# Performance work log

Hardware: AMD Instinct MI355X
Metric: run time of the kernel (lower is better)

## Reference

```python
import jax, jax.numpy as jnp
import numpy as np

D = 256      # dim_model (hardcoded in module)
H = 8        # n_head
HD = 64      # num_neuron (per-head dim)
NL = 5       # number of transformer blocks
FF = 4 * D   # FFN hidden
VOCAB = 32000
OUT = 4096
B = 32
S = 512
LN_EPS = 1e-5


def layer_norm(x, s, b):
    m = jnp.mean(x, axis=-1, keepdims=True)
    v = jnp.mean(jnp.square(x - m), axis=-1, keepdims=True)
    return (x - m) * jax.lax.rsqrt(v + LN_EPS) * s + b


def setup_inputs() -> dict:
    key = jax.random.key(0)
    ks = jax.random.split(key, 12)
    sd = 0.02
    return {
        "x": jax.random.randint(ks[0], (B, S), 0, VOCAB),
        "emb": jax.random.normal(ks[1], (VOCAB, D), jnp.float32) * sd,
        "wq": jax.random.normal(ks[2], (NL, D, H * HD), jnp.float32) * sd,
        "bq": jnp.zeros((NL, H * HD), jnp.float32),
        "wk": jax.random.normal(ks[3], (NL, D, H * HD), jnp.float32) * sd,
        "bk": jnp.zeros((NL, H * HD), jnp.float32),
        "wv": jax.random.normal(ks[4], (NL, D, H * HD), jnp.float32) * sd,
        "bv": jnp.zeros((NL, H * HD), jnp.float32),
        "wo": jax.random.normal(ks[5], (NL, H * HD, D), jnp.float32) * sd,
        "bo": jnp.zeros((NL, D), jnp.float32),
        "ln1_s": jnp.ones((NL, D), jnp.float32),
        "ln1_b": jnp.zeros((NL, D), jnp.float32),
        "w1": jax.random.normal(ks[6], (NL, D, FF), jnp.float32) * sd,
        "b1": jnp.zeros((NL, FF), jnp.float32),
        "w2": jax.random.normal(ks[7], (NL, FF, D), jnp.float32) * sd,
        "b2": jnp.zeros((NL, D), jnp.float32),
        "ln2_s": jnp.ones((NL, D), jnp.float32),
        "ln2_b": jnp.zeros((NL, D), jnp.float32),
        "ow": jax.random.normal(ks[8], (D, OUT), jnp.float32) * sd,
        "ob": jnp.zeros((OUT,), jnp.float32),
    }


def positional_encoding(seq_len):
    pos = jnp.arange(seq_len, dtype=jnp.float32)[:, None]          # [S,1]
    div = 10000.0 ** (jnp.arange(0, D, 2, dtype=jnp.float32) / D)  # [D/2]
    ang = pos / div                                                # [S,D/2]
    pe = jnp.zeros((seq_len, D), jnp.float32)
    pe = pe.at[:, 0::2].set(jnp.sin(ang))
    pe = pe.at[:, 1::2].set(jnp.cos(ang))
    return pe


def reference(x, emb, wq, bq, wk, bk, wv, bv, wo, bo,
              ln1_s, ln1_b, w1, b1, w2, b2, ln2_s, ln2_b, ow, ob):
    Bx, Sx = x.shape
    h = emb[x] + positional_encoding(Sx)[None]          # [B,S,D]
    causal = jnp.tril(jnp.ones((Sx, Sx), bool))         # [S,S]
    scale = 1.0 / jnp.sqrt(jnp.float32(HD))
    for i in range(NL):
        q = (h @ wq[i] + bq[i]).reshape(Bx, Sx, H, HD)
        k = (h @ wk[i] + bk[i]).reshape(Bx, Sx, H, HD)
        v = (h @ wv[i] + bv[i]).reshape(Bx, Sx, H, HD)
        scores = jnp.einsum('bqhd,bkhd->bhqk', q, k) * scale
        scores = jnp.where(causal, scores, -jnp.inf)
        attn_w = jax.nn.softmax(scores, axis=-1)
        o = jnp.einsum('bhqk,bkhd->bqhd', attn_w, v).reshape(Bx, Sx, H * HD)
        attn = o @ wo[i] + bo[i]
        h = layer_norm(h + attn, ln1_s[i], ln1_b[i])
        ff = jax.nn.relu(h @ w1[i] + b1[i]) @ w2[i] + b2[i]
        h = layer_norm(h + ff, ln2_s[i], ln2_b[i])
    return h @ ow + ob
```

## Files before the change

kernel.cpp:

```cpp
#include <hip/hip_runtime.h>

#define BB   32
#define SS   512
#define DD   256
#define HH   8
#define HDIM 64
#define NLAYER 5
#define FFD  1024
#define OUTD 4096
#define QN   512
#define BS   (BB*SS)

typedef short bf16x8 __attribute__((ext_vector_type(8)));
typedef float f32x4  __attribute__((ext_vector_type(4)));

__device__ __forceinline__ ushort f2bf(float f) {
    union { float f; unsigned u; } c; c.f = f;
    unsigned u = c.u;
    return (ushort)((u + 0x7fffu + ((u >> 16) & 1u)) >> 16);
}
__device__ __forceinline__ float bf2f(unsigned b) {
    union { unsigned u; float f; } c; c.u = b << 16;
    return c.f;
}

__global__ __launch_bounds__(256) void embed_pe_kernel(
        const int* __restrict__ x, const float* __restrict__ emb,
        float* __restrict__ h, ushort* __restrict__ hb) {
    int t = blockIdx.x;
    int d = threadIdx.x;
    int pos = t % SS;
    int tok = x[t];
    float e = emb[(size_t)tok * DD + d];
    float expo = -(float)(d & ~1) / (float)DD;
    float ang = (float)pos * powf(10000.0f, expo);
    float pe = (d & 1) ? cosf(ang) : sinf(ang);
    float val = e + pe;
    h[(size_t)t * DD + d] = val;
    hb[(size_t)t * DD + d] = f2bf(val);
}

__global__ __launch_bounds__(256) void convw_kernel(
        const float* __restrict__ W, ushort* __restrict__ Wt, int K, int N) {
    __shared__ float t[32][33];
    const int tid = threadIdx.x;
    const int tx = tid & 31, ty = tid >> 5;
    const int n0 = blockIdx.x * 32, k0 = blockIdx.y * 32;
#pragma unroll
    for (int i = 0; i < 4; ++i)
        t[ty + i * 8][tx] = W[(size_t)(k0 + ty + i * 8) * N + n0 + tx];
    __syncthreads();
#pragma unroll
    for (int i = 0; i < 4; ++i)
        Wt[(size_t)(n0 + ty + i * 8) * K + k0 + tx] = f2bf(t[tx][ty + i * 8]);
}

template<bool RELU, bool OBF>
__global__ __launch_bounds__(256) void gemm_mfma_kernel(
        const ushort* __restrict__ A, const ushort* __restrict__ Bt,
        const float* __restrict__ bias, void* __restrict__ Cout,
        int M, int N, int K) {
    __shared__ ushort sA[128 * 32];
    __shared__ ushort sB[128 * 32];

    const int tid  = threadIdx.x;
    const int lane = tid & 63;
    const int wave = tid >> 6;
    const int wr   = wave >> 1;
    const int wc   = wave & 1;
    const int fr   = lane & 15;
    const int fq   = lane >> 4;
    const int m0 = blockIdx.y * 128;
    const int n0 = blockIdx.x * 128;

    f32x4 acc[4][4];
#pragma unroll
    for (int mi = 0; mi < 4; ++mi)
#pragma unroll
        for (int ni = 0; ni < 4; ++ni)
            acc[mi][ni] = (f32x4){0.0f, 0.0f, 0.0f, 0.0f};

    for (int k0 = 0; k0 < K; k0 += 32) {
#pragma unroll
        for (int it = 0; it < 2; ++it) {
            const int gi  = tid + it * 256;
            const int row = gi >> 2, g = gi & 3;
            const int gs  = g ^ ((row >> 1) & 3);
            const uint4 av = *reinterpret_cast<const uint4*>(
                A + (size_t)(m0 + row) * K + k0 + g * 8);
            *reinterpret_cast<uint4*>(&sA[row * 32 + gs * 8]) = av;
            const uint4 bv = *reinterpret_cast<const uint4*>(
                Bt + (size_t)(n0 + row) * K + k0 + g * 8);
            *reinterpret_cast<uint4*>(&sB[row * 32 + gs * 8]) = bv;
        }
        __syncthreads();

        bf16x8 af[4], bfr[4];
#pragma unroll
        for (int mi = 0; mi < 4; ++mi) {
            const int row = wr * 64 + mi * 16 + fr;
            const int gs  = fq ^ ((row >> 1) & 3);
            af[mi] = *reinterpret_cast<const bf16x8*>(&sA[row * 32 + gs * 8]);
        }
#pragma unroll
        for (int ni = 0; ni < 4; ++ni) {
            const int row = wc * 64 + ni * 16 + fr;
            const int gs  = fq ^ ((row >> 1) & 3);
            bfr[ni] = *reinterpret_cast<const bf16x8*>(&sB[row * 32 + gs * 8]);
        }
#pragma unroll
        for (int mi = 0; mi < 4; ++mi)
#pragma unroll
            for (int ni = 0; ni < 4; ++ni)
                acc[mi][ni] = __builtin_amdgcn_mfma_f32_16x16x32_bf16(
                    af[mi], bfr[ni], acc[mi][ni], 0, 0, 0);
        __syncthreads();
    }

#pragma unroll
    for (int ni = 0; ni < 4; ++ni) {
        const int col = n0 + wc * 64 + ni * 16 + fr;
        const float bv = bias[col];
#pragma unroll
        for (int mi = 0; mi < 4; ++mi) {
#pragma unroll
            for (int r = 0; r < 4; ++r) {
                const int row = m0 + wr * 64 + mi * 16 + fq * 4 + r;
                float v = acc[mi][ni][r] + bv;
                if (RELU) v = fmaxf(v, 0.0f);
                if (OBF)
                    ((ushort*)Cout)[(size_t)row * N + col] = f2bf(v);
                else
                    ((float*)Cout)[(size_t)row * N + col] = v;
            }
        }
    }
}

__global__ __launch_bounds__(256) void flash_attn_kernel(
        const ushort* __restrict__ q, const ushort* __restrict__ k,
        const ushort* __restrict__ v, ushort* __restrict__ o) {
    const int qt  = blockIdx.x;
    const int hh  = blockIdx.y;
    const int b   = blockIdx.z;
    const int tid = threadIdx.x;
    const int l   = tid & 63;
    const int w   = tid >> 6;
    const int lf  = l & 15;
    const int lg  = l >> 4;

    __shared__ ushort Qs[64 * 64];
    __shared__ ushort Ks[64 * 64];
    __shared__ ushort Vt[64 * 64];
    __shared__ ushort Ps[64 * 64];

    const size_t qbase = ((size_t)(b * SS + qt * 64)) * QN + hh * HDIM;

#pragma unroll
    for (int it = 0; it < 2; ++it) {
        int gi = tid + it * 256;
        int row = gi >> 3, g = gi & 7;
        uint4 val = *reinterpret_cast<const uint4*>(
            q + qbase + (size_t)row * QN + g * 8);
        *reinterpret_cast<uint4*>(&Qs[row * 64 + ((g ^ (row & 7)) << 3)]) = val;
    }

    f32x4 o_acc[4];
    float m_i[4], l_i[4];
#pragma unroll
    for (int r = 0; r < 4; ++r) { m_i[r] = -3.0e38f; l_i[r] = 0.0f; }
#pragma unroll
    for (int ni = 0; ni < 4; ++ni) o_acc[ni] = (f32x4){0.f, 0.f, 0.f, 0.f};

    const int vkv  = l;
    const int vgd  = w * 2;

    for (int kt = 0; kt <= qt; ++kt) {
        const size_t kbase = ((size_t)(b * SS + kt * 64)) * QN + hh * HDIM;
#pragma unroll
        for (int it = 0; it < 2; ++it) {
            int gi = tid + it * 256;
            int row = gi >> 3, g = gi & 7;
            uint4 val = *reinterpret_cast<const uint4*>(
                k + kbase + (size_t)row * QN + g * 8);
            *reinterpret_cast<uint4*>(&Ks[row * 64 + ((g ^ (row & 7)) << 3)]) = val;
        }
#pragma unroll
        for (int sel = 0; sel < 2; ++sel) {
            const int gd = vgd + sel;
            uint4 raw = *reinterpret_cast<const uint4*>(
                v + kbase + (size_t)vkv * QN + gd * 8);
            unsigned e[4] = {raw.x, raw.y, raw.z, raw.w};
#pragma unroll
            for (int j = 0; j < 8; ++j) {
                int d = gd * 8 + j;
                ushort val = (ushort)((e[j >> 1] >> ((j & 1) * 16)) & 0xffff);
                Vt[d * 64 + (((vkv >> 3) ^ (d & 7)) << 3) + (vkv & 7)] = val;
            }
        }
        __syncthreads();

        f32x4 st[4];
#pragma unroll
        for (int ni = 0; ni < 4; ++ni) st[ni] = (f32x4){0.f, 0.f, 0.f, 0.f};
        const int arow = w * 16 + lf;
#pragma unroll
        for (int ks = 0; ks < 2; ++ks) {
            bf16x8 aq = *reinterpret_cast<const bf16x8*>(
                &Qs[arow * 64 + (((ks * 4 + lg) ^ (arow & 7)) << 3)]);
#pragma unroll
            for (int ni = 0; ni < 4; ++ni) {
                const int brow = ni * 16 + lf;
                bf16x8 bk = *reinterpret_cast<const bf16x8*>(
                    &Ks[brow * 64 + (((ks * 4 + lg) ^ (brow & 7)) << 3)]);
                st[ni] = __builtin_amdgcn_mfma_f32_16x16x32_bf16(aq, bk, st[ni], 0, 0, 0);
            }
        }
#pragma unroll
        for (int ni = 0; ni < 4; ++ni) st[ni] *= 0.125f;

        if (kt == qt) {
#pragma unroll
            for (int ni = 0; ni < 4; ++ni)
#pragma unroll
                for (int r = 0; r < 4; ++r)
                    if (16 * ni + lf > w * 16 + 4 * lg + r) st[ni][r] = -1.0e30f;
        }

#pragma unroll
        for (int r = 0; r < 4; ++r) {
            float mx = fmaxf(fmaxf(st[0][r], st[1][r]), fmaxf(st[2][r], st[3][r]));
#pragma unroll
            for (int off = 1; off < 16; off <<= 1)
                mx = fmaxf(mx, __shfl_xor(mx, off, 64));
            float mnew = fmaxf(m_i[r], mx);
            float alpha = __expf(m_i[r] - mnew);
            float sum = 0.0f;
#pragma unroll
            for (int ni = 0; ni < 4; ++ni) {
                float p = __expf(st[ni][r] - mnew);
                st[ni][r] = p;
                sum += p;
            }
#pragma unroll
            for (int off = 1; off < 16; off <<= 1)
                sum += __shfl_xor(sum, off, 64);
            m_i[r] = mnew;
            l_i[r] = l_i[r] * alpha + sum;
#pragma unroll
            for (int ni = 0; ni < 4; ++ni) o_acc[ni][r] *= alpha;
        }

#pragma unroll
        for (int r = 0; r < 4; ++r) {
            const int qr = w * 16 + 4 * lg + r;
#pragma unroll
            for (int ni = 0; ni < 4; ++ni) {
                const int kvc = 16 * ni + lf;
                Ps[qr * 64 + (((kvc >> 3) ^ (qr & 7)) << 3) + (kvc & 7)] =
                    f2bf(st[ni][r]);
            }
        }
        asm volatile("s_waitcnt lgkmcnt(0)" ::: "memory");
        __builtin_amdgcn_sched_barrier(0);

#pragma unroll
        for (int ks = 0; ks < 2; ++ks) {
            bf16x8 pa = *reinterpret_cast<const bf16x8*>(
                &Ps[arow * 64 + (((ks * 4 + lg) ^ (arow & 7)) << 3)]);
#pragma unroll
            for (int ni = 0; ni < 4; ++ni) {
                const int drow = ni * 16 + lf;
                bf16x8 vb = *reinterpret_cast<const bf16x8*>(
                    &Vt[drow * 64 + (((ks * 4 + lg) ^ (drow & 7)) << 3)]);
                o_acc[ni] = __builtin_amdgcn_mfma_f32_16x16x32_bf16(pa, vb, o_acc[ni], 0, 0, 0);
            }
        }
        __syncthreads();
    }

#pragma unroll
    for (int r = 0; r < 4; ++r) {
        const float invl = 1.0f / l_i[r];
        const int qrow = w * 16 + 4 * lg + r;
#pragma unroll
        for (int ni = 0; ni < 4; ++ni)
            o[qbase + (size_t)qrow * QN + 16 * ni + lf] =
                f2bf(o_acc[ni][r] * invl);
    }
}

__global__ __launch_bounds__(256) void add_ln_kernel(
        float* __restrict__ h, const float* __restrict__ delta,
        const float* __restrict__ sc, const float* __restrict__ bi,
        ushort* __restrict__ hb) {
    const int t = blockIdx.x;
    const int d = threadIdx.x;
    __shared__ float p1[4], p2[4];
    const size_t idx = (size_t)t * DD + d;
    float val = h[idx] + delta[idx];
    float s = val;
#pragma unroll
    for (int off = 1; off < 64; off <<= 1) s += __shfl_xor(s, off, 64);
    if ((d & 63) == 0) p1[d >> 6] = s;
    __syncthreads();
    float mean = (p1[0] + p1[1] + p1[2] + p1[3]) * (1.0f / DD);
    float dv = val - mean;
    float vs = dv * dv;
#pragma unroll
    for (int off = 1; off < 64; off <<= 1) vs += __shfl_xor(vs, off, 64);
    if ((d & 63) == 0) p2[d >> 6] = vs;
    __syncthreads();
    float inv = rsqrtf((p2[0] + p2[1] + p2[2] + p2[3]) * (1.0f / DD) + 1e-5f);
    float r = dv * inv * sc[d] + bi[d];
    h[idx] = r;
    hb[idx] = f2bf(r);
}

extern "C" void kernel_launch(void* const* d_in, const int* in_sizes, int n_in,
                              void* d_out, int out_size, void* d_ws, size_t ws_size,
                              hipStream_t stream) {
    (void)in_sizes; (void)n_in; (void)out_size; (void)ws_size;

    const int*   x    = (const int*)d_in[0];
    const float* emb  = (const float*)d_in[1];
    const float* wq   = (const float*)d_in[2];
    const float* bq   = (const float*)d_in[3];
    const float* wk   = (const float*)d_in[4];
    const float* bk   = (const float*)d_in[5];
    const float* wv   = (const float*)d_in[6];
    const float* bv   = (const float*)d_in[7];
    const float* wo   = (const float*)d_in[8];
    const float* bo   = (const float*)d_in[9];
    const float* ln1s = (const float*)d_in[10];
    const float* ln1b = (const float*)d_in[11];
    const float* w1   = (const float*)d_in[12];
    const float* b1   = (const float*)d_in[13];
    const float* w2   = (const float*)d_in[14];
    const float* b2   = (const float*)d_in[15];
    const float* ln2s = (const float*)d_in[16];
    const float* ln2b = (const float*)d_in[17];
    const float* ow   = (const float*)d_in[18];
    const float* ob   = (const float*)d_in[19];

    char* ws = (char*)d_ws;
    float*  h   = (float*)ws;   ws += (size_t)BS * DD * 4;
    ushort* hbf = (ushort*)ws;  ws += (size_t)BS * DD * 2;
    ushort* qb  = (ushort*)ws;  ws += (size_t)BS * QN * 2;
    ushort* kb  = (ushort*)ws;  ws += (size_t)BS * QN * 2;
    ushort* vb  = (ushort*)ws;  ws += (size_t)BS * QN * 2;
    float*  t2  = (float*)ws;   ws += (size_t)BS * DD * 4;
    ushort* wqt = (ushort*)ws;  ws += (size_t)NLAYER * QN * DD * 2;
    ushort* wkt = (ushort*)ws;  ws += (size_t)NLAYER * QN * DD * 2;
    ushort* wvt = (ushort*)ws;  ws += (size_t)NLAYER * QN * DD * 2;
    ushort* wot = (ushort*)ws;  ws += (size_t)NLAYER * DD * QN * 2;
    ushort* w1t = (ushort*)ws;  ws += (size_t)NLAYER * FFD * DD * 2;
    ushort* w2t = (ushort*)ws;  ws += (size_t)NLAYER * DD * FFD * 2;
    ushort* owt = (ushort*)ws;  ws += (size_t)OUTD * DD * 2;
    ushort* ao  = qb;
    ushort* ffh = kb;

    for (int i = 0; i < NLAYER; ++i) {
        convw_kernel<<<dim3(QN / 32, DD / 32), 256, 0, stream>>>(
            wq + (size_t)i * DD * QN, wqt + (size_t)i * QN * DD, DD, QN);
        convw_kernel<<<dim3(QN / 32, DD / 32), 256, 0, stream>>>(
            wk + (size_t)i * DD * QN, wkt + (size_t)i * QN * DD, DD, QN);
        convw_kernel<<<dim3(QN / 32, DD / 32), 256, 0, stream>>>(
            wv + (size_t)i * DD * QN, wvt + (size_t)i * QN * DD, DD, QN);
        convw_kernel<<<dim3(DD / 32, QN / 32), 256, 0, stream>>>(
            wo + (size_t)i * QN * DD, wot + (size_t)i * DD * QN, QN, DD);
        convw_kernel<<<dim3(FFD / 32, DD / 32), 256, 0, stream>>>(
            w1 + (size_t)i * DD * FFD, w1t + (size_t)i * FFD * DD, DD, FFD);
        convw_kernel<<<dim3(DD / 32, FFD / 32), 256, 0, stream>>>(
            w2 + (size_t)i * FFD * DD, w2t + (size_t)i * DD * FFD, FFD, DD);
    }
    convw_kernel<<<dim3(OUTD / 32, DD / 32), 256, 0, stream>>>(ow, owt, DD, OUTD);

    embed_pe_kernel<<<BS, 256, 0, stream>>>(x, emb, h, hbf);

    for (int i = 0; i < NLAYER; ++i) {
        dim3 gq(QN / 128, BS / 128);
        gemm_mfma_kernel<false, true><<<gq, 256, 0, stream>>>(
            hbf, wqt + (size_t)i * QN * DD, bq + i * QN, qb, BS, QN, DD);
        gemm_mfma_kernel<false, true><<<gq, 256, 0, stream>>>(
            hbf, wkt + (size_t)i * QN * DD, bk + i * QN, kb, BS, QN, DD);
        gemm_mfma_kernel<false, true><<<gq, 256, 0, stream>>>(
            hbf, wvt + (size_t)i * QN * DD, bv + i * QN, vb, BS, QN, DD);

        flash_attn_kernel<<<dim3(SS / 64, HH, BB), 256, 0, stream>>>(qb, kb, vb, ao);

        gemm_mfma_kernel<false, false><<<dim3(DD / 128, BS / 128), 256, 0, stream>>>(
            ao, wot + (size_t)i * DD * QN, bo + i * DD, t2, BS, DD, QN);
        add_ln_kernel<<<BS, 256, 0, stream>>>(h, t2, ln1s + i * DD, ln1b + i * DD, hbf);

        gemm_mfma_kernel<true, true><<<dim3(FFD / 128, BS / 128), 256, 0, stream>>>(
            hbf, w1t + (size_t)i * FFD * DD, b1 + i * FFD, ffh, BS, FFD, DD);
        gemm_mfma_kernel<false, false><<<dim3(DD / 128, BS / 128), 256, 0, stream>>>(
            ffh, w2t + (size_t)i * DD * FFD, b2 + i * DD, t2, BS, DD, FFD);
        add_ln_kernel<<<BS, 256, 0, stream>>>(h, t2, ln2s + i * DD, ln2b + i * DD, hbf);
    }

    gemm_mfma_kernel<false, false><<<dim3(OUTD / 128, BS / 128), 256, 0, stream>>>(
        hbf, owt, ob, (float*)d_out, BS, OUTD, DD);
}
```

Before: 1.443 ms.

## Fuse QKV GEMMs, fuse output GEMMs with add+LayerNorm, prefetch tiles, pre-transpose V

Merges the three Q/K/V projections into one GEMM launch over concatenated weights, and writes V transposed so the attention kernel can load it with vector copies instead of a scalar transpose. The Wo and W2 projections are fused with the residual add and LayerNorm in a new full-row GEMM kernel, which removes the t2 round trip and the separate add_ln launches. All GEMM and attention loops gain register prefetch of the next tile, overlapping global loads with MFMA work. The embedding now uses fast-math exp/sin/cos. The fused LN kernel runs only 256 blocks with 16 accumulators per lane, so occupancy may drop.

```diff
diff --git a/kernel.cpp b/kernel.cpp
--- a/kernel.cpp
+++ b/kernel.cpp
@@ -33,8 +33,8 @@
     int tok = x[t];
     float e = emb[(size_t)tok * DD + d];
     float expo = -(float)(d & ~1) / (float)DD;
-    float ang = (float)pos * powf(10000.0f, expo);
-    float pe = (d & 1) ? cosf(ang) : sinf(ang);
+    float ang = (float)pos * __expf(expo * 9.210340371976184f);
+    float pe = (d & 1) ? __cosf(ang) : __sinf(ang);
     float val = e + pe;
     h[(size_t)t * DD + d] = val;
     hb[(size_t)t * DD + d] = f2bf(val);
@@ -73,6 +73,10 @@
     const int m0 = blockIdx.y * 128;
     const int n0 = blockIdx.x * 128;
 
+    const int strow = tid >> 2;
+    const int stg   = tid & 3;
+    const int stgs  = stg ^ ((strow >> 1) & 3);
+
     f32x4 acc[4][4];
 #pragma unroll
     for (int mi = 0; mi < 4; ++mi)
@@ -80,20 +84,31 @@
         for (int ni = 0; ni < 4; ++ni)
             acc[mi][ni] = (f32x4){0.0f, 0.0f, 0.0f, 0.0f};
 
+    uint4 apre[2], bpre[2];
+#pragma unroll
+    for (int it = 0; it < 2; ++it) {
+        apre[it] = *reinterpret_cast<const uint4*>(
+            A + (size_t)(m0 + strow + it * 64) * K + stg * 8);
+        bpre[it] = *reinterpret_cast<const uint4*>(
+            Bt + (size_t)(n0 + strow + it * 64) * K + stg * 8);
+    }
+
     for (int k0 = 0; k0 < K; k0 += 32) {
 #pragma unroll
         for (int it = 0; it < 2; ++it) {
-            const int gi  = tid + it * 256;
-            const int row = gi >> 2, g = gi & 3;
-            const int gs  = g ^ ((row >> 1) & 3);
-            const uint4 av = *reinterpret_cast<const uint4*>(
-                A + (size_t)(m0 + row) * K + k0 + g * 8);
-            *reinterpret_cast<uint4*>(&sA[row * 32 + gs * 8]) = av;
-            const uint4 bv = *reinterpret_cast<const uint4*>(
-                Bt + (size_t)(n0 + row) * K + k0 + g * 8);
-            *reinterpret_cast<uint4*>(&sB[row * 32 + gs * 8]) = bv;
-        }
-        __syncthreads();
+            *reinterpret_cast<uint4*>(&sA[(strow + it * 64) * 32 + stgs * 8]) = apre[it];
+            *reinterpret_cast<uint4*>(&sB[(strow + it * 64) * 32 + stgs * 8]) = bpre[it];
+        }
+        __syncthreads();
+        if (k0 + 32 < K) {
+#pragma unroll
+            for (int it = 0; it < 2; ++it) {
+                apre[it] = *reinterpret_cast<const uint4*>(
+                    A + (size_t)(m0 + strow + it * 64) * K + k0 + 32 + stg * 8);
+                bpre[it] = *reinterpret_cast<const uint4*>(
+                    Bt + (size_t)(n0 + strow + it * 64) * K + k0 + 32 + stg * 8);
+            }
+        }
 
         bf16x8 af[4], bfr[4];
 #pragma unroll
@@ -137,9 +152,214 @@
     }
 }
 
+__global__ __launch_bounds__(256) void gemm_qkv_kernel(
+        const ushort* __restrict__ A, const ushort* __restrict__ Bt,
+        const float* __restrict__ bq, const float* __restrict__ bk,
+        const float* __restrict__ bv,
+        ushort* __restrict__ qo, ushort* __restrict__ ko,
+        ushort* __restrict__ vt) {
+    __shared__ ushort sA[128 * 32];
+    __shared__ ushort sB[128 * 32];
+
+    const int tid  = threadIdx.x;
+    const int lane = tid & 63;
+    const int wave = tid >> 6;
+    const int wr   = wave >> 1;
+    const int wc   = wave & 1;
+    const int fr   = lane & 15;
+    const int fq   = lane >> 4;
+    const int m0 = blockIdx.y * 128;
+    const int n0 = blockIdx.x * 128;
+    const int K  = DD;
+
+    const int strow = tid >> 2;
+    const int stg   = tid & 3;
+    const int stgs  = stg ^ ((strow >> 1) & 3);
+
+    f32x4 acc[4][4];
+#pragma unroll
+    for (int mi = 0; mi < 4; ++mi)
+#pragma unroll
+        for (int ni = 0; ni < 4; ++ni)
+            acc[mi][ni] = (f32x4){0.0f, 0.0f, 0.0f, 0.0f};
+
+    uint4 apre[2], bpre[2];
+#pragma unroll
+    for (int it = 0; it < 2; ++it) {
+        apre[it] = *reinterpret_cast<const uint4*>(
+            A + (size_t)(m0 + strow + it * 64) * K + stg * 8);
+        bpre[it] = *reinterpret_cast<const uint4*>(
+            Bt + (size_t)(n0 + strow + it * 64) * K + stg * 8);
+    }
+
+    for (int k0 = 0; k0 < K; k0 += 32) {
+#pragma unroll
+        for (int it = 0; it < 2; ++it) {
+            *reinterpret_cast<uint4*>(&sA[(strow + it * 64) * 32 + stgs * 8]) = apre[it];
+            *reinterpret_cast<uint4*>(&sB[(strow + it * 64) * 32 + stgs * 8]) = bpre[it];
+        }
+        __syncthreads();
+        if (k0 + 32 < K) {
+#pragma unroll
+            for (int it = 0; it < 2; ++it) {
+                apre[it] = *reinterpret_cast<const uint4*>(
+                    A + (size_t)(m0 + strow + it * 64) * K + k0 + 32 + stg * 8);
+                bpre[it] = *reinterpret_cast<const uint4*>(
+                    Bt + (size_t)(n0 + strow + it * 64) * K + k0 + 32 + stg * 8);
+            }
+        }
+
+        bf16x8 af[4], bfr[4];
+#pragma unroll
+        for (int mi = 0; mi < 4; ++mi) {
+            const int row = wr * 64 + mi * 16 + fr;
+            const int gs  = fq ^ ((row >> 1) & 3);
+            af[mi] = *reinterpret_cast<const bf16x8*>(&sA[row * 32 + gs * 8]);
+        }
+#pragma unroll
+        for (int ni = 0; ni < 4; ++ni) {
+            const int row = wc * 64 + ni * 16 + fr;
+            const int gs  = fq ^ ((row >> 1) & 3);
+            bfr[ni] = *reinterpret_cast<const bf16x8*>(&sB[row * 32 + gs * 8]);
+        }
+#pragma unroll
+        for (int mi = 0; mi < 4; ++mi)
+#pragma unroll
+            for (int ni = 0; ni < 4; ++ni)
+                acc[mi][ni] = __builtin_amdgcn_mfma_f32_16x16x32_bf16(
+                    af[mi], bfr[ni], acc[mi][ni], 0, 0, 0);
+        __syncthreads();
+    }
+
+    const int which = n0 >> 9;
+    if (which < 2) {
+        ushort* out = which ? ko : qo;
+        const float* bias = which ? bk : bq;
+#pragma unroll
+        for (int ni = 0; ni < 4; ++ni) {
+            const int col = (n0 + wc * 64 + ni * 16 + fr) & 511;
+            const float bvv = bias[col];
+#pragma unroll
+            for (int mi = 0; mi < 4; ++mi)
+#pragma unroll
+                for (int r = 0; r < 4; ++r) {
+                    const int row = m0 + wr * 64 + mi * 16 + fq * 4 + r;
+                    out[(size_t)row * QN + col] = f2bf(acc[mi][ni][r] + bvv);
+                }
+        }
+    } else {
+#pragma unroll
+        for (int ni = 0; ni < 4; ++ni) {
+            const int col = (n0 + wc * 64 + ni * 16 + fr) & 511;
+            const float bvv = bv[col];
+#pragma unroll
+            for (int mi = 0; mi < 4; ++mi) {
+                const int row_base = m0 + wr * 64 + mi * 16 + fq * 4;
+                ushort4 pk = make_ushort4(
+                    f2bf(acc[mi][ni][0] + bvv), f2bf(acc[mi][ni][1] + bvv),
+                    f2bf(acc[mi][ni][2] + bvv), f2bf(acc[mi][ni][3] + bvv));
+                *reinterpret_cast<ushort4*>(vt + (size_t)col * BS + row_base) = pk;
+            }
+        }
+    }
+}
+
+__global__ __launch_bounds__(256) void gemm_ln_kernel(
+        const ushort* __restrict__ A, const ushort* __restrict__ Bt,
+        const float* __restrict__ bias, float* __restrict__ h,
+        ushort* __restrict__ hb, const float* __restrict__ sc,
+        const float* __restrict__ bi, int K) {
+    __shared__ ushort sA[64 * 32];
+    __shared__ ushort sB[256 * 32];
+
+    const int tid  = threadIdx.x;
+    const int lane = tid & 63;
+    const int w    = tid >> 6;
+    const int lf   = lane & 15;
+    const int fq   = lane >> 4;
+    const int m0   = blockIdx.x * 64;
+
+    const int strow = tid >> 2;
+    const int stg   = tid & 3;
+    const int stgs  = stg ^ ((strow >> 1) & 3);
+
+    f32x4 acc[16];
+#pragma unroll
+    for (int ni = 0; ni < 16; ++ni) acc[ni] = (f32x4){0.f, 0.f, 0.f, 0.f};
+
+    uint4 apre;
+    uint4 bpre[4];
+    apre = *reinterpret_cast<const uint4*>(A + (size_t)(m0 + strow) * K + stg * 8);
+#pragma unroll
+    for (int it = 0; it < 4; ++it)
+        bpre[it] = *reinterpret_cast<const uint4*>(
+            Bt + (size_t)(strow + it * 64) * K + stg * 8);
+
+    for (int k0 = 0; k0 < K; k0 += 32) {
+        *reinterpret_cast<uint4*>(&sA[strow * 32 + stgs * 8]) = apre;
+#pragma unroll
+        for (int it = 0; it < 4; ++it)
+            *reinterpret_cast<uint4*>(&sB[(strow + it * 64) * 32 + stgs * 8]) = bpre[it];
+        __syncthreads();
+        if (k0 + 32 < K) {
+            apre = *reinterpret_cast<const uint4*>(
+                A + (size_t)(m0 + strow) * K + k0 + 32 + stg * 8);
+#pragma unroll
+            for (int it = 0; it < 4; ++it)
+                bpre[it] = *reinterpret_cast<const uint4*>(
+                    Bt + (size_t)(strow + it * 64) * K + k0 + 32 + stg * 8);
+        }
+
+        const int arow = w * 16 + lf;
+        const bf16x8 af = *reinterpret_cast<const bf16x8*>(
+            &sA[arow * 32 + ((fq ^ ((arow >> 1) & 3)) << 3)]);
+#pragma unroll
+        for (int ni = 0; ni < 16; ++ni) {
+            const int brow = ni * 16 + lf;
+            const bf16x8 bfr = *reinterpret_cast<const bf16x8*>(
+                &sB[brow * 32 + ((fq ^ ((brow >> 1) & 3)) << 3)]);
+            acc[ni] = __builtin_amdgcn_mfma_f32_16x16x32_bf16(af, bfr, acc[ni], 0, 0, 0);
+        }
+        __syncthreads();
+    }
+
+#pragma unroll
+    for (int r = 0; r < 4; ++r) {
+        const int row = m0 + w * 16 + fq * 4 + r;
+        float tmp[16];
+        float sum = 0.0f;
+#pragma unroll
+        for (int ni = 0; ni < 16; ++ni) {
+            const int col = ni * 16 + lf;
+            float v = acc[ni][r] + bias[col] + h[(size_t)row * DD + col];
+            tmp[ni] = v;
+            sum += v;
+        }
+#pragma unroll
+        for (int off = 1; off < 16; off <<= 1) sum += __shfl_xor(sum, off, 64);
+        const float mean = sum * (1.0f / DD);
+        float vs = 0.0f;
+#pragma unroll
+        for (int ni = 0; ni < 16; ++ni) {
+            float d = tmp[ni] - mean;
+            vs += d * d;
+        }
+#pragma unroll
+        for (int off = 1; off < 16; off <<= 1) vs += __shfl_xor(vs, off, 64);
+        const float inv = rsqrtf(vs * (1.0f / DD) + 1e-5f);
+#pragma unroll
+        for (int ni = 0; ni < 16; ++ni) {
+            const int col = ni * 16 + lf;
+            float res = (tmp[ni] - mean) * inv * sc[col] + bi[col];
+            h[(size_t)row * DD + col] = res;
+            hb[(size_t)row * DD + col] = f2bf(res);
+        }
+    }
+}
+
 __global__ __launch_bounds__(256) void flash_attn_kernel(
         const ushort* __restrict__ q, const ushort* __restrict__ k,
-        const ushort* __restrict__ v, ushort* __restrict__ o) {
+        const ushort* __restrict__ vt, ushort* __restrict__ o) {
     const int qt  = blockIdx.x;
     const int hh  = blockIdx.y;
     const int b   = blockIdx.z;
@@ -155,6 +375,7 @@
     __shared__ ushort Ps[64 * 64];
 
     const size_t qbase = ((size_t)(b * SS + qt * 64)) * QN + hh * HDIM;
+    const ushort* vbase = vt + (size_t)(hh * HDIM) * BS + (size_t)b * SS;
 
 #pragma unroll
     for (int it = 0; it < 2; ++it) {
@@ -165,6 +386,9 @@
         *reinterpret_cast<uint4*>(&Qs[row * 64 + ((g ^ (row & 7)) << 3)]) = val;
     }
 
+    const int srow[2] = { tid >> 3, (tid + 256) >> 3 };
+    const int sg      = tid & 7;
+
     f32x4 o_acc[4];
     float m_i[4], l_i[4];
 #pragma unroll
@@ -172,33 +396,38 @@
 #pragma unroll
     for (int ni = 0; ni < 4; ++ni) o_acc[ni] = (f32x4){0.f, 0.f, 0.f, 0.f};
 
-    const int vkv  = l;
-    const int vgd  = w * 2;
+    uint4 kreg[2], vreg[2];
+    {
+        const size_t kbase = ((size_t)(b * SS)) * QN + hh * HDIM;
+#pragma unroll
+        for (int it = 0; it < 2; ++it) {
+            kreg[it] = *reinterpret_cast<const uint4*>(
+                k + kbase + (size_t)srow[it] * QN + sg * 8);
+            vreg[it] = *reinterpret_cast<const uint4*>(
+                vbase + (size_t)srow[it] * BS + sg * 8);
+        }
+    }
 
     for (int kt = 0; kt <= qt; ++kt) {
-        const size_t kbase = ((size_t)(b * SS + kt * 64)) * QN + hh * HDIM;
 #pragma unroll
         for (int it = 0; it < 2; ++it) {
-            int gi = tid + it * 256;
-            int row = gi >> 3, g = gi & 7;
-            uint4 val = *reinterpret_cast<const uint4*>(
-                k + kbase + (size_t)row * QN + g * 8);
-            *reinterpret_cast<uint4*>(&Ks[row * 64 + ((g ^ (row & 7)) << 3)]) = val;
-        }
-#pragma unroll
-        for (int sel = 0; sel < 2; ++sel) {
-            const int gd = vgd + sel;
-            uint4 raw = *reinterpret_cast<const uint4*>(
-                v + kbase + (size_t)vkv * QN + gd * 8);
-            unsigned e[4] = {raw.x, raw.y, raw.z, raw.w};
-#pragma unroll
-            for (int j = 0; j < 8; ++j) {
-                int d = gd * 8 + j;
-                ushort val = (ushort)((e[j >> 1] >> ((j & 1) * 16)) & 0xffff);
-                Vt[d * 64 + (((vkv >> 3) ^ (d & 7)) << 3) + (vkv & 7)] = val;
-            }
-        }
-        __syncthreads();
+            *reinterpret_cast<uint4*>(
+                &Ks[srow[it] * 64 + ((sg ^ (srow[it] & 7)) << 3)]) = kreg[it];
+            *reinterpret_cast<uint4*>(
+                &Vt[srow[it] * 64 + ((sg ^ (srow[it] & 7)) << 3)]) = vreg[it];
+        }
+        __syncthreads();
+
+        if (kt < qt) {
+            const size_t kbase = ((size_t)(b * SS + (kt + 1) * 64)) * QN + hh * HDIM;
+#pragma unroll
+            for (int it = 0; it < 2; ++it) {
+                kreg[it] = *reinterpret_cast<const uint4*>(
+                    k + kbase + (size_t)srow[it] * QN + sg * 8);
+                vreg[it] = *reinterpret_cast<const uint4*>(
+                    vbase + (kt + 1) * 64 + (size_t)srow[it] * BS + sg * 8);
+            }
+        }
 
         f32x4 st[4];
 #pragma unroll
@@ -288,33 +517,6 @@
             o[qbase + (size_t)qrow * QN + 16 * ni + lf] =
                 f2bf(o_acc[ni][r] * invl);
     }
-}
-
-__global__ __launch_bounds__(256) void add_ln_kernel(
-        float* __restrict__ h, const float* __restrict__ delta,
-        const float* __restrict__ sc, const float* __restrict__ bi,
-        ushort* __restrict__ hb) {
-    const int t = blockIdx.x;
-    const int d = threadIdx.x;
-    __shared__ float p1[4], p2[4];
-    const size_t idx = (size_t)t * DD + d;
-    float val = h[idx] + delta[idx];
-    float s = val;
-#pragma unroll
-    for (int off = 1; off < 64; off <<= 1) s += __shfl_xor(s, off, 64);
-    if ((d & 63) == 0) p1[d >> 6] = s;
-    __syncthreads();
-    float mean = (p1[0] + p1[1] + p1[2] + p1[3]) * (1.0f / DD);
-    float dv = val - mean;
-    float vs = dv * dv;
-#pragma unroll
-    for (int off = 1; off < 64; off <<= 1) vs += __shfl_xor(vs, off, 64);
-    if ((d & 63) == 0) p2[d >> 6] = vs;
-    __syncthreads();
-    float inv = rsqrtf((p2[0] + p2[1] + p2[2] + p2[3]) * (1.0f / DD) + 1e-5f);
-    float r = dv * inv * sc[d] + bi[d];
-    h[idx] = r;
-    hb[idx] = f2bf(r);
 }
 
 extern "C" void kernel_launch(void* const* d_in, const int* in_sizes, int n_in,
@@ -344,29 +546,27 @@
     const float* ob   = (const float*)d_in[19];
 
     char* ws = (char*)d_ws;
-    float*  h   = (float*)ws;   ws += (size_t)BS * DD * 4;
-    ushort* hbf = (ushort*)ws;  ws += (size_t)BS * DD * 2;
-    ushort* qb  = (ushort*)ws;  ws += (size_t)BS * QN * 2;
-    ushort* kb  = (ushort*)ws;  ws += (size_t)BS * QN * 2;
-    ushort* vb  = (ushort*)ws;  ws += (size_t)BS * QN * 2;
-    float*  t2  = (float*)ws;   ws += (size_t)BS * DD * 4;
-    ushort* wqt = (ushort*)ws;  ws += (size_t)NLAYER * QN * DD * 2;
-    ushort* wkt = (ushort*)ws;  ws += (size_t)NLAYER * QN * DD * 2;
-    ushort* wvt = (ushort*)ws;  ws += (size_t)NLAYER * QN * DD * 2;
-    ushort* wot = (ushort*)ws;  ws += (size_t)NLAYER * DD * QN * 2;
-    ushort* w1t = (ushort*)ws;  ws += (size_t)NLAYER * FFD * DD * 2;
-    ushort* w2t = (ushort*)ws;  ws += (size_t)NLAYER * DD * FFD * 2;
-    ushort* owt = (ushort*)ws;  ws += (size_t)OUTD * DD * 2;
-    ushort* ao  = qb;
-    ushort* ffh = kb;
+    float*  h     = (float*)ws;   ws += (size_t)BS * DD * 4;
+    ushort* hbf   = (ushort*)ws;  ws += (size_t)BS * DD * 2;
+    ushort* qb    = (ushort*)ws;  ws += (size_t)BS * QN * 2;
+    ushort* kb    = (ushort*)ws;  ws += (size_t)BS * QN * 2;
+    ushort* vbt   = (ushort*)ws;  ws += (size_t)QN * BS * 2;
+    ushort* wqkvt = (ushort*)ws;  ws += (size_t)NLAYER * 3 * QN * DD * 2;
+    ushort* wot   = (ushort*)ws;  ws += (size_t)NLAYER * DD * QN * 2;
+    ushort* w1t   = (ushort*)ws;  ws += (size_t)NLAYER * FFD * DD * 2;
+    ushort* w2t   = (ushort*)ws;  ws += (size_t)NLAYER * DD * FFD * 2;
+    ushort* owt   = (ushort*)ws;  ws += (size_t)OUTD * DD * 2;
+    ushort* ao    = qb;
+    ushort* ffh   = kb;
 
     for (int i = 0; i < NLAYER; ++i) {
+        ushort* base = wqkvt + (size_t)i * 3 * QN * DD;
         convw_kernel<<<dim3(QN / 32, DD / 32), 256, 0, stream>>>(
-            wq + (size_t)i * DD * QN, wqt + (size_t)i * QN * DD, DD, QN);
+            wq + (size_t)i * DD * QN, base, DD, QN);
         convw_kernel<<<dim3(QN / 32, DD / 32), 256, 0, stream>>>(
-            wk + (size_t)i * DD * QN, wkt + (size_t)i * QN * DD, DD, QN);
+            wk + (size_t)i * DD * QN, base + (size_t)QN * DD, DD, QN);
         convw_kernel<<<dim3(QN / 32, DD / 32), 256, 0, stream>>>(
-            wv + (size_t)i * DD * QN, wvt + (size_t)i * QN * DD, DD, QN);
+            wv + (size_t)i * DD * QN, base + (size_t)2 * QN * DD, DD, QN);
         convw_kernel<<<dim3(DD / 32, QN / 32), 256, 0, stream>>>(
             wo + (size_t)i * QN * DD, wot + (size_t)i * DD * QN, QN, DD);
         convw_kernel<<<dim3(FFD / 32, DD / 32), 256, 0, stream>>>(
@@ -379,25 +579,22 @@
     embed_pe_kernel<<<BS, 256, 0, stream>>>(x, emb, h, hbf);
 
     for (int i = 0; i < NLAYER; ++i) {
-        dim3 gq(QN / 128, BS / 128);
-        gemm_mfma_kernel<false, true><<<gq, 256, 0, stream>>>(
-            hbf, wqt + (size_t)i * QN * DD, bq + i * QN, qb, BS, QN, DD);
-        gemm_mfma_kernel<false, true><<<gq, 256, 0, stream>>>(
-            hbf, wkt + (size_t)i * QN * DD, bk + i * QN, kb, BS, QN, DD);
-        gemm_mfma_kernel<false, true><<<gq, 256, 0, stream>>>(
-            hbf, wvt + (size_t)i * QN * DD, bv + i * QN, vb, BS, QN, DD);
-
-        flash_attn_kernel<<<dim3(SS / 64, HH, BB), 256, 0, stream>>>(qb, kb, vb, ao);
-
-        gemm_mfma_kernel<false, false><<<dim3(DD / 128, BS / 128), 256, 0, stream>>>(
-            ao, wot + (size_t)i * DD * QN, bo + i * DD, t2, BS, DD, QN);
-        add_ln_kernel<<<BS, 256, 0, stream>>>(h, t2, ln1s + i * DD, ln1b + i * DD, hbf);
+        gemm_qkv_kernel<<<dim3(12, BS / 128), 256, 0, stream>>>(
+            hbf, wqkvt + (size_t)i * 3 * QN * DD,
+            bq + i * QN, bk + i * QN, bv + i * QN, qb, kb, vbt);
+
+        flash_attn_kernel<<<dim3(SS / 64, HH, BB), 256, 0, stream>>>(qb, kb, vbt, ao);
+
+        gemm_ln_kernel<<<BS / 64, 256, 0, stream>>>(
+            ao, wot + (size_t)i * DD * QN, bo + i * DD, h, hbf,
+            ln1s + i * DD, ln1b + i * DD, QN);
 
         gemm_mfma_kernel<true, true><<<dim3(FFD / 128, BS / 128), 256, 0, stream>>>(
             hbf, w1t + (size_t)i * FFD * DD, b1 + i * FFD, ffh, BS, FFD, DD);
-        gemm_mfma_kernel<false, false><<<dim3(DD / 128, BS / 128), 256, 0, stream>>>(
-            ffh, w2t + (size_t)i * DD * FFD, b2 + i * DD, t2, BS, DD, FFD);
-        add_ln_kernel<<<BS, 256, 0, stream>>>(h, t2, ln2s + i * DD, ln2b + i * DD, hbf);
+
+        gemm_ln_kernel<<<BS / 64, 256, 0, stream>>>(
+            ffh, w2t + (size_t)i * DD * FFD, b2 + i * DD, h, hbf,
+            ln2s + i * DD, ln2b + i * DD, FFD);
     }
 
     gemm_mfma_kernel<false, false><<<dim3(OUTD / 128, BS / 128), 256, 0, stream>>>(
```

Measured after the change: 2.196 ms. 1.52x slower.
